# Kernel tuning notes

Hardware: AMD Instinct MI355X
Metric: run time of the kernel (lower is better)

Reference implementation:

```python
import jax, jax.numpy as jnp
import numpy as np

B, T, E, H = 4, 1024, 1024, 16
HS = E // H  # 64
EPS = 1e-5


def layernorm(x, g, b):
    mu = jnp.mean(x, axis=-1, keepdims=True)
    var = jnp.mean((x - mu) ** 2, axis=-1, keepdims=True)
    return (x - mu) * jax.lax.rsqrt(var + EPS) * g + b


def setup_inputs() -> dict:
    key = jax.random.key(0)
    ks = jax.random.split(key, 10)
    s = 0.02
    return {
        "v": jax.random.normal(ks[0], (B, T, E), jnp.float32),
        "k": jax.random.normal(ks[1], (B, T, E), jnp.float32),
        "q": jax.random.normal(ks[2], (B, T, E), jnp.float32),
        "ln_g": jnp.ones((E,), jnp.float32),
        "ln_b": jnp.zeros((E,), jnp.float32),
        # per-head projection weights stacked: [E, H, HS] (x @ W form)
        "Wq": jax.random.normal(ks[3], (E, H, HS), jnp.float32) * s,
        "Wk": jax.random.normal(ks[4], (E, H, HS), jnp.float32) * s,
        "Wv": jax.random.normal(ks[5], (E, H, HS), jnp.float32) * s,
        "Wp": jax.random.normal(ks[6], (E, E), jnp.float32) * s,
        "bp": jnp.zeros((E,), jnp.float32),
    }


def reference(v, k, q, ln_g, ln_b, Wq, Wk, Wv, Wp, bp):
    # shared LayerNorm applied to all three streams
    vn = layernorm(v, ln_g, ln_b)
    kn = layernorm(k, ln_g, ln_b)
    qn = layernorm(q, ln_g, ln_b)
    # batched per-head projections: [B,T,E] x [E,H,HS] -> [B,H,T,HS]
    qh = jnp.einsum("bte,ehd->bhtd", qn, Wq)
    kh = jnp.einsum("bte,ehd->bhtd", kn, Wk)
    vh = jnp.einsum("bte,ehd->bhtd", vn, Wv)
    # NOTE: original scales by C^-0.5 where C = embedding_dim (not head_size)
    scale = jnp.float32(E) ** -0.5
    scores = jnp.einsum("bhtd,bhsd->bhts", qh, kh) * scale  # [B,H,T,T]
    causal = jnp.tril(jnp.ones((T, T), bool))
    scores = jnp.where(causal, scores, jnp.finfo(scores.dtype).min)
    w = jax.nn.softmax(scores, axis=-1)
    out = jnp.einsum("bhts,bhsd->bhtd", w, vh)  # [B,H,T,HS]
    out = out.transpose(0, 2, 1, 3).reshape(B, T, E)  # concat heads
    return out @ Wp + bp
```

## Files before the change

kernel.cpp:

```cpp
#include <hip/hip_runtime.h>
#include <stdint.h>

#define B_ 4
#define T_ 1024
#define E_ 1024
#define H_ 16
#define HS_ 64
#define BT_ 4096

typedef unsigned short u16;
typedef __attribute__((ext_vector_type(8))) short bf16x8;
typedef __attribute__((ext_vector_type(4))) float f32x4;

__device__ __forceinline__ u16 f2bf(float f) {
    unsigned u = __float_as_uint(f);
    u += 0x7fff + ((u >> 16) & 1);
    return (u16)(u >> 16);
}

__device__ __forceinline__ void gll16(const void* g, void* l) {
    __builtin_amdgcn_global_load_lds(
        (const __attribute__((address_space(1))) unsigned int*)g,
        (__attribute__((address_space(3))) unsigned int*)l, 16, 0, 0);
}

__global__ __launch_bounds__(256) void ln_all(
    const float* __restrict__ v, const float* __restrict__ k,
    const float* __restrict__ q, const float* __restrict__ g,
    const float* __restrict__ b,
    u16* __restrict__ vn, u16* __restrict__ kn, u16* __restrict__ qn)
{
    int row = blockIdx.x;
    int which = row >> 12;
    int r = row & 4095;
    const float* src = which == 0 ? v : which == 1 ? k : q;
    u16* dst = which == 0 ? vn : which == 1 ? kn : qn;

    int t = threadIdx.x;
    float4 x = ((const float4*)(src + (size_t)r * E_))[t];
    float s  = x.x + x.y + x.z + x.w;
    float ss = x.x * x.x + x.y * x.y + x.z * x.z + x.w * x.w;
    for (int off = 32; off; off >>= 1) {
        s  += __shfl_down(s, off, 64);
        ss += __shfl_down(ss, off, 64);
    }
    __shared__ float red[8];
    int w = t >> 6, l = t & 63;
    if (l == 0) { red[w] = s; red[4 + w] = ss; }
    __syncthreads();
    float fs  = red[0] + red[1] + red[2] + red[3];
    float fss = red[4] + red[5] + red[6] + red[7];
    float mu  = fs * (1.0f / E_);
    float var = fss * (1.0f / E_) - mu * mu;
    float rstd = rsqrtf(var + 1e-5f);

    float4 gg = ((const float4*)g)[t];
    float4 bb = ((const float4*)b)[t];
    ushort4 o;
    o.x = f2bf((x.x - mu) * rstd * gg.x + bb.x);
    o.y = f2bf((x.y - mu) * rstd * gg.y + bb.y);
    o.z = f2bf((x.z - mu) * rstd * gg.z + bb.z);
    o.w = f2bf((x.w - mu) * rstd * gg.w + bb.w);
    ((ushort4*)(dst + (size_t)r * E_))[t] = o;
}

__global__ __launch_bounds__(256) void wcast_t(
    const float* __restrict__ wq, const float* __restrict__ wk,
    const float* __restrict__ wv, const float* __restrict__ wp,
    u16* __restrict__ tq, u16* __restrict__ tk,
    u16* __restrict__ tv, u16* __restrict__ tp)
{
    int z = blockIdx.z;
    const float* src = z == 0 ? wq : z == 1 ? wk : z == 2 ? wv : wp;
    u16* dst = z == 0 ? tq : z == 1 ? tk : z == 2 ? tv : tp;
    __shared__ float tile[32][33];
    int n0 = blockIdx.x * 32, k0 = blockIdx.y * 32;
    int tx = threadIdx.x & 31, ty = threadIdx.x >> 5;
    for (int i = 0; i < 4; i++)
        tile[ty + i * 8][tx] = src[(size_t)(k0 + ty + i * 8) * E_ + n0 + tx];
    __syncthreads();
    for (int i = 0; i < 4; i++)
        dst[(size_t)(n0 + ty + i * 8) * E_ + k0 + tx] = f2bf(tile[tx][ty + i * 8]);
}

__global__ __launch_bounds__(256) void gemm64(
    const u16* __restrict__ X0, const u16* __restrict__ X1, const u16* __restrict__ X2,
    const u16* __restrict__ W0, const u16* __restrict__ W1, const u16* __restrict__ W2,
    u16* __restrict__ qh, u16* __restrict__ kh, u16* __restrict__ vt,
    float* __restrict__ outF, const float* __restrict__ bias, int fin)
{
    __shared__ __attribute__((aligned(16))) char smem[24576];
    int z = blockIdx.z;
    int mode = fin ? 3 : z;
    const u16* X  = z == 0 ? X0 : z == 1 ? X1 : X2;
    const u16* Wt = z == 0 ? W0 : z == 1 ? W1 : W2;

    const int K = 1024;
    int n0 = blockIdx.x * 128, m0 = blockIdx.y * 64;
    int t = threadIdx.x, w = t >> 6, l = t & 63;
    int lr = l & 15, lg = l >> 4, wm = w >> 1, wn = w & 1;

    f32x4 acc[2][4];
    f32x4 zero = {0.f, 0.f, 0.f, 0.f};
    for (int i = 0; i < 2; i++)
        for (int j = 0; j < 4; j++) acc[i][j] = zero;

    const char* Xb = (const char*)X + (size_t)m0 * 2048;
    const char* Wb = (const char*)Wt + (size_t)n0 * 2048;

    int srow = l >> 2;
    int scol = ((l & 3) ^ ((l >> 3) & 3)) * 16;
    int arow = w * 16 + srow;
    int brow0 = (w * 2) * 16 + srow;
    int brow1 = (w * 2 + 1) * 16 + srow;

    auto stage = [&](int k0, int buf) {
        int kb = k0 * 2;
        gll16(Xb + (size_t)arow * 2048 + kb + scol,
              smem + buf * 4096 + w * 1024 + l * 16);
        gll16(Wb + (size_t)brow0 * 2048 + kb + scol,
              smem + 8192 + buf * 8192 + (w * 2) * 1024 + l * 16);
        gll16(Wb + (size_t)brow1 * 2048 + kb + scol,
              smem + 8192 + buf * 8192 + (w * 2 + 1) * 1024 + l * 16);
    };

    stage(0, 0);
    __syncthreads();
    int b = 0;
    int swr = (lr >> 1) & 3;
    for (int k0 = 0; k0 < K; k0 += 32) {
        if (k0 + 32 < K) stage(k0 + 32, b ^ 1);
        const u16* As = (const u16*)(smem + b * 4096);
        const u16* Bs = (const u16*)(smem + 8192 + b * 8192);
        bf16x8 af[2], bfr[4];
        for (int i = 0; i < 2; i++)
            af[i] = *(const bf16x8*)&As[(wm * 32 + i * 16 + lr) * 32 + (lg ^ swr) * 8];
        for (int j = 0; j < 4; j++)
            bfr[j] = *(const bf16x8*)&Bs[(wn * 64 + j * 16 + lr) * 32 + (lg ^ swr) * 8];
        for (int i = 0; i < 2; i++)
            for (int j = 0; j < 4; j++)
                acc[i][j] = __builtin_amdgcn_mfma_f32_16x16x32_bf16(
                    af[i], bfr[j], acc[i][j], 0, 0, 0);
        __syncthreads();
        b ^= 1;
    }

    if (mode == 3) {
        for (int i = 0; i < 2; i++)
            for (int j = 0; j < 4; j++)
                for (int r = 0; r < 4; r++) {
                    int row = m0 + wm * 32 + i * 16 + lg * 4 + r;
                    int col = n0 + wn * 64 + j * 16 + lr;
                    outF[(size_t)row * E_ + col] = acc[i][j][r] + bias[col];
                }
    } else if (mode < 2) {
        u16* outB = mode == 0 ? qh : kh;
        float sc = mode == 0 ? 0.03125f : 1.0f;
        for (int i = 0; i < 2; i++)
            for (int j = 0; j < 4; j++)
                for (int r = 0; r < 4; r++) {
                    int row = m0 + wm * 32 + i * 16 + lg * 4 + r;
                    int col = n0 + wn * 64 + j * 16 + lr;
                    int bb = row >> 10, tt = row & 1023;
                    int hh = col >> 6, dd = col & 63;
                    outB[(((size_t)(bb * H_ + hh)) * T_ + tt) * HS_ + dd] =
                        f2bf(acc[i][j][r] * sc);
                }
    } else {
        __syncthreads();
        u16* Tt = (u16*)smem + w * 2560;
        for (int i = 0; i < 2; i++)
            for (int j = 0; j < 4; j++)
                for (int r = 0; r < 4; r++)
                    Tt[(j * 16 + lr) * 40 + i * 16 + lg * 4 + r] = f2bf(acc[i][j][r]);
        int bb = m0 >> 10;
        int tbase = (m0 & 1023) + wm * 32;
        int hh = (n0 + wn * 64) >> 6;
        u16* outV = vt + ((size_t)(bb * H_ + hh)) * HS_ * T_;
        int dl = l >> 2, tc = l & 3;
        for (int u = 0; u < 4; u++) {
            int d = u * 16 + dl;
            bf16x8 vv = *(const bf16x8*)&Tt[d * 40 + tc * 8];
            *(bf16x8*)&outV[(size_t)d * T_ + tbase + tc * 8] = vv;
        }
    }
}

__global__ __launch_bounds__(256) void attn(
    const u16* __restrict__ Qh, const u16* __restrict__ Kh,
    const u16* __restrict__ Vt, u16* __restrict__ Out)
{
    int qt = 15 - blockIdx.x;
    int bh = blockIdx.y;
    int b = bh >> 4, h = bh & 15;
    int t = threadIdx.x, w = t >> 6, l = t & 63;
    int lr = l & 15, lg = l >> 4;
    int sw = lr & 7;

    __shared__ __attribute__((aligned(16))) u16 Ks[2][4096];
    __shared__ __attribute__((aligned(16))) u16 Vs[2][4096];
    __shared__ __attribute__((aligned(16))) u16 Ps[4][1024];

    const char* Kb = (const char*)(Kh + (size_t)bh * T_ * HS_);
    const char* Vb = (const char*)(Vt + (size_t)bh * HS_ * T_);
    const u16*  Qb = Qh + (size_t)bh * T_ * HS_;

    int ris = l >> 3;
    int csw = (l & 7) ^ ris;

    int qrow = qt * 64 + w * 16 + lr;
    bf16x8 qf0 = *(const bf16x8*)&Qb[qrow * 64 + lg * 8];
    bf16x8 qf1 = *(const bf16x8*)&Qb[qrow * 64 + 32 + lg * 8];

    f32x4 zero = {0.f, 0.f, 0.f, 0.f};
    f32x4 o[4];
    float m[4], psum[4];
    for (int i = 0; i < 4; i++) o[i] = zero;
    for (int r = 0; r < 4; r++) { m[r] = -1e30f; psum[r] = 0.f; }

    int nkv = qt + 1;

    auto stageKV = [&](int kt2, int bsel) {
        int kv0 = kt2 * 64;
        for (int j = 0; j < 2; j++) {
            int seg = w * 2 + j;
            int row = seg * 8 + ris;
            gll16(Kb + (size_t)(kv0 + row) * 128 + csw * 16,
                  (char*)Ks[bsel] + seg * 1024);
            gll16(Vb + (size_t)row * 2048 + (size_t)kv0 * 2 + csw * 16,
                  (char*)Vs[bsel] + seg * 1024);
        }
    };

    stageKV(0, 0);
    __syncthreads();
    int bsel = 0;

    for (int kt = 0; kt < nkv; kt++) {
        if (kt + 1 < nkv) stageKV(kt + 1, bsel ^ 1);

        int kv0 = kt * 64;
        const u16* Kl = Ks[bsel];
        const u16* Vl = Vs[bsel];

        f32x4 s[4];
        __builtin_amdgcn_s_setprio(1);
        for (int kf = 0; kf < 4; kf++) {
            int key = kf * 16 + lr;
            bf16x8 bk0 = *(const bf16x8*)&Kl[key * 64 + (lg ^ sw) * 8];
            bf16x8 bk1 = *(const bf16x8*)&Kl[key * 64 + ((lg + 4) ^ sw) * 8];
            s[kf] = __builtin_amdgcn_mfma_f32_16x16x32_bf16(qf0, bk0, zero, 0, 0, 0);
            s[kf] = __builtin_amdgcn_mfma_f32_16x16x32_bf16(qf1, bk1, s[kf], 0, 0, 0);
        }
        __builtin_amdgcn_s_setprio(0);

        if (kt == qt) {
            for (int kf = 0; kf < 4; kf++)
                for (int r = 0; r < 4; r++) {
                    int key = kv0 + kf * 16 + lr;
                    int qr  = qt * 64 + w * 16 + lg * 4 + r;
                    if (key > qr) s[kf][r] = -1e30f;
                }
        }

        float pmr[4];
        for (int r = 0; r < 4; r++)
            pmr[r] = fmaxf(fmaxf(s[0][r], s[1][r]), fmaxf(s[2][r], s[3][r]));
        bool ok = (pmr[0] <= m[0] + 8.f) & (pmr[1] <= m[1] + 8.f) &
                  (pmr[2] <= m[2] + 8.f) & (pmr[3] <= m[3] + 8.f);
        if (!__all(ok)) {
            for (int r = 0; r < 4; r++) {
                float mt = pmr[r];
                for (int off = 1; off < 16; off <<= 1)
                    mt = fmaxf(mt, __shfl_xor(mt, off, 64));
                float mn = fmaxf(m[r], mt);
                float al = __expf(m[r] - mn);
                m[r] = mn;
                psum[r] *= al;
                for (int nf = 0; nf < 4; nf++) o[nf][r] *= al;
            }
        }

        for (int kf = 0; kf < 4; kf++)
            for (int r = 0; r < 4; r++) {
                float p = __expf(s[kf][r] - m[r]);
                psum[r] += p;
                int row = lg * 4 + r;
                int ch  = (kf * 2 + (lr >> 3)) ^ (row & 7);
                Ps[w][row * 64 + ch * 8 + sw] = f2bf(p);
            }

        __builtin_amdgcn_s_setprio(1);
        for (int ks = 0; ks < 2; ks++) {
            bf16x8 pa = *(const bf16x8*)&Ps[w][lr * 64 + ((ks * 4 + lg) ^ sw) * 8];
            for (int nf = 0; nf < 4; nf++) {
                int d = nf * 16 + lr;
                bf16x8 bv = *(const bf16x8*)&Vl[d * 64 + ((ks * 4 + lg) ^ sw) * 8];
                o[nf] = __builtin_amdgcn_mfma_f32_16x16x32_bf16(pa, bv, o[nf], 0, 0, 0);
            }
        }
        __builtin_amdgcn_s_setprio(0);
        __syncthreads();
        bsel ^= 1;
    }

    for (int r = 0; r < 4; r++)
        for (int off = 1; off < 16; off <<= 1)
            psum[r] += __shfl_xor(psum[r], off, 64);

    for (int nf = 0; nf < 4; nf++)
        for (int r = 0; r < 4; r++) {
            int row = qt * 64 + w * 16 + lg * 4 + r;
            int col = h * 64 + nf * 16 + lr;
            Out[((size_t)(b * T_ + row)) * E_ + col] = f2bf(o[nf][r] / psum[r]);
        }
}

extern "C" void kernel_launch(void* const* d_in, const int* in_sizes, int n_in,
                              void* d_out, int out_size, void* d_ws, size_t ws_size,
                              hipStream_t stream) {
    const float* v  = (const float*)d_in[0];
    const float* k  = (const float*)d_in[1];
    const float* q  = (const float*)d_in[2];
    const float* g  = (const float*)d_in[3];
    const float* be = (const float*)d_in[4];
    const float* Wq = (const float*)d_in[5];
    const float* Wk = (const float*)d_in[6];
    const float* Wv = (const float*)d_in[7];
    const float* Wp = (const float*)d_in[8];
    const float* bp = (const float*)d_in[9];
    float* out = (float*)d_out;

    char* ws = (char*)d_ws;
    u16* qh  = (u16*)(ws);
    u16* kh  = (u16*)(ws + (8u  << 20));
    u16* vt  = (u16*)(ws + (16u << 20));
    u16* qn  = (u16*)(ws + (24u << 20));
    u16* kn  = (u16*)(ws + (32u << 20));
    u16* vn  = (u16*)(ws + (40u << 20));
    u16* wtq = (u16*)(ws + (48u << 20));
    u16* wtk = (u16*)(ws + (50u << 20));
    u16* wtv = (u16*)(ws + (52u << 20));
    u16* wtp = (u16*)(ws + (54u << 20));
    u16* ao  = (u16*)(ws + (24u << 20));

    hipLaunchKernelGGL(wcast_t, dim3(32, 32, 4), dim3(256), 0, stream,
                       Wq, Wk, Wv, Wp, wtq, wtk, wtv, wtp);
    hipLaunchKernelGGL(ln_all, dim3(3 * BT_), dim3(256), 0, stream,
                       v, k, q, g, be, vn, kn, qn);
    hipLaunchKernelGGL(gemm64, dim3(8, 64, 3), dim3(256), 0, stream,
                       qn, kn, vn, wtq, wtk, wtv, qh, kh, vt,
                       (float*)nullptr, (const float*)nullptr, 0);
    hipLaunchKernelGGL(attn, dim3(16, 64), dim3(256), 0, stream,
                       qh, kh, vt, ao);
    hipLaunchKernelGGL(gemm64, dim3(8, 64, 1), dim3(256), 0, stream,
                       ao, ao, ao, wtp, wtp, wtp,
                       (u16*)nullptr, (u16*)nullptr, (u16*)nullptr, out, bp, 1);
}
```

Baseline: 237.9 us.

## Enlarge GEMM tiles to 128x128, double attention query tile, swizzle block order

The projection GEMM now computes 128x128 output tiles per block instead of 64x128, which doubles the reuse of each staged weight tile and halves the grid. The attention kernel handles 128 query rows per block, with each wave holding two 16-row query fragments, so every staged K/V tile feeds twice as many MFMAs. Both kernels remap block IDs through a swizzle to improve L2 locality. In exchange, register pressure and LDS use rise, the grids shrink (possibly underfilling the CUs), and causal load balance becomes coarser.

```diff
diff --git a/kernel.cpp b/kernel.cpp
--- a/kernel.cpp
+++ b/kernel.cpp
@@ -83,45 +83,49 @@
         dst[(size_t)(n0 + ty + i * 8) * E_ + k0 + tx] = f2bf(tile[tx][ty + i * 8]);
 }
 
-__global__ __launch_bounds__(256) void gemm64(
+__global__ __launch_bounds__(256) void gemm128(
     const u16* __restrict__ X0, const u16* __restrict__ X1, const u16* __restrict__ X2,
     const u16* __restrict__ W0, const u16* __restrict__ W1, const u16* __restrict__ W2,
     u16* __restrict__ qh, u16* __restrict__ kh, u16* __restrict__ vt,
     float* __restrict__ outF, const float* __restrict__ bias, int fin)
 {
-    __shared__ __attribute__((aligned(16))) char smem[24576];
-    int z = blockIdx.z;
-    int mode = fin ? 3 : z;
-    const u16* X  = z == 0 ? X0 : z == 1 ? X1 : X2;
-    const u16* Wt = z == 0 ? W0 : z == 1 ? W1 : W2;
+    __shared__ __attribute__((aligned(16))) char smem[36864];
+    int lid = blockIdx.x + 8 * (blockIdx.y + 32 * blockIdx.z);
+    int cpx = fin ? 32 : 96;
+    int swz = (lid & 7) * cpx + (lid >> 3);
+    int bx = swz & 7;
+    int by = (swz >> 3) & 31;
+    int bz = swz >> 8;
+
+    int mode = fin ? 3 : bz;
+    const u16* X  = bz == 0 ? X0 : bz == 1 ? X1 : X2;
+    const u16* Wt = bz == 0 ? W0 : bz == 1 ? W1 : W2;
 
     const int K = 1024;
-    int n0 = blockIdx.x * 128, m0 = blockIdx.y * 64;
+    int n0 = bx * 128, m0 = by * 128;
     int t = threadIdx.x, w = t >> 6, l = t & 63;
     int lr = l & 15, lg = l >> 4, wm = w >> 1, wn = w & 1;
 
-    f32x4 acc[2][4];
+    f32x4 acc[4][4];
     f32x4 zero = {0.f, 0.f, 0.f, 0.f};
-    for (int i = 0; i < 2; i++)
+    for (int i = 0; i < 4; i++)
         for (int j = 0; j < 4; j++) acc[i][j] = zero;
 
     const char* Xb = (const char*)X + (size_t)m0 * 2048;
     const char* Wb = (const char*)Wt + (size_t)n0 * 2048;
 
-    int srow = l >> 2;
     int scol = ((l & 3) ^ ((l >> 3) & 3)) * 16;
-    int arow = w * 16 + srow;
-    int brow0 = (w * 2) * 16 + srow;
-    int brow1 = (w * 2 + 1) * 16 + srow;
 
     auto stage = [&](int k0, int buf) {
         int kb = k0 * 2;
-        gll16(Xb + (size_t)arow * 2048 + kb + scol,
-              smem + buf * 4096 + w * 1024 + l * 16);
-        gll16(Wb + (size_t)brow0 * 2048 + kb + scol,
-              smem + 8192 + buf * 8192 + (w * 2) * 1024 + l * 16);
-        gll16(Wb + (size_t)brow1 * 2048 + kb + scol,
-              smem + 8192 + buf * 8192 + (w * 2 + 1) * 1024 + l * 16);
+        for (int j = 0; j < 2; j++) {
+            int seg = w * 2 + j;
+            int row = seg * 16 + (l >> 2);
+            gll16(Xb + (size_t)row * 2048 + kb + scol,
+                  smem + buf * 8192 + seg * 1024 + l * 16);
+            gll16(Wb + (size_t)row * 2048 + kb + scol,
+                  smem + 16384 + buf * 8192 + seg * 1024 + l * 16);
+        }
     };
 
     stage(0, 0);
@@ -130,14 +134,14 @@
     int swr = (lr >> 1) & 3;
     for (int k0 = 0; k0 < K; k0 += 32) {
         if (k0 + 32 < K) stage(k0 + 32, b ^ 1);
-        const u16* As = (const u16*)(smem + b * 4096);
-        const u16* Bs = (const u16*)(smem + 8192 + b * 8192);
-        bf16x8 af[2], bfr[4];
-        for (int i = 0; i < 2; i++)
-            af[i] = *(const bf16x8*)&As[(wm * 32 + i * 16 + lr) * 32 + (lg ^ swr) * 8];
+        const u16* As = (const u16*)(smem + b * 8192);
+        const u16* Bs = (const u16*)(smem + 16384 + b * 8192);
+        bf16x8 af[4], bfr[4];
+        for (int i = 0; i < 4; i++)
+            af[i] = *(const bf16x8*)&As[(wm * 64 + i * 16 + lr) * 32 + (lg ^ swr) * 8];
         for (int j = 0; j < 4; j++)
             bfr[j] = *(const bf16x8*)&Bs[(wn * 64 + j * 16 + lr) * 32 + (lg ^ swr) * 8];
-        for (int i = 0; i < 2; i++)
+        for (int i = 0; i < 4; i++)
             for (int j = 0; j < 4; j++)
                 acc[i][j] = __builtin_amdgcn_mfma_f32_16x16x32_bf16(
                     af[i], bfr[j], acc[i][j], 0, 0, 0);
@@ -146,20 +150,20 @@
     }
 
     if (mode == 3) {
-        for (int i = 0; i < 2; i++)
+        for (int i = 0; i < 4; i++)
             for (int j = 0; j < 4; j++)
                 for (int r = 0; r < 4; r++) {
-                    int row = m0 + wm * 32 + i * 16 + lg * 4 + r;
+                    int row = m0 + wm * 64 + i * 16 + lg * 4 + r;
                     int col = n0 + wn * 64 + j * 16 + lr;
                     outF[(size_t)row * E_ + col] = acc[i][j][r] + bias[col];
                 }
     } else if (mode < 2) {
         u16* outB = mode == 0 ? qh : kh;
         float sc = mode == 0 ? 0.03125f : 1.0f;
-        for (int i = 0; i < 2; i++)
+        for (int i = 0; i < 4; i++)
             for (int j = 0; j < 4; j++)
                 for (int r = 0; r < 4; r++) {
-                    int row = m0 + wm * 32 + i * 16 + lg * 4 + r;
+                    int row = m0 + wm * 64 + i * 16 + lg * 4 + r;
                     int col = n0 + wn * 64 + j * 16 + lr;
                     int bb = row >> 10, tt = row & 1023;
                     int hh = col >> 6, dd = col & 63;
@@ -167,20 +171,19 @@
                         f2bf(acc[i][j][r] * sc);
                 }
     } else {
-        __syncthreads();
-        u16* Tt = (u16*)smem + w * 2560;
-        for (int i = 0; i < 2; i++)
+        u16* Tt = (u16*)smem + w * 4608;
+        for (int i = 0; i < 4; i++)
             for (int j = 0; j < 4; j++)
                 for (int r = 0; r < 4; r++)
-                    Tt[(j * 16 + lr) * 40 + i * 16 + lg * 4 + r] = f2bf(acc[i][j][r]);
+                    Tt[(j * 16 + lr) * 72 + i * 16 + lg * 4 + r] = f2bf(acc[i][j][r]);
         int bb = m0 >> 10;
-        int tbase = (m0 & 1023) + wm * 32;
+        int tbase = (m0 & 1023) + wm * 64;
         int hh = (n0 + wn * 64) >> 6;
         u16* outV = vt + ((size_t)(bb * H_ + hh)) * HS_ * T_;
-        int dl = l >> 2, tc = l & 3;
-        for (int u = 0; u < 4; u++) {
-            int d = u * 16 + dl;
-            bf16x8 vv = *(const bf16x8*)&Tt[d * 40 + tc * 8];
+        int dl = l >> 3, tc = l & 7;
+        for (int u = 0; u < 8; u++) {
+            int d = u * 8 + dl;
+            bf16x8 vv = *(const bf16x8*)&Tt[d * 72 + tc * 8];
             *(bf16x8*)&outV[(size_t)d * T_ + tbase + tc * 8] = vv;
         }
     }
@@ -190,8 +193,10 @@
     const u16* __restrict__ Qh, const u16* __restrict__ Kh,
     const u16* __restrict__ Vt, u16* __restrict__ Out)
 {
-    int qt = 15 - blockIdx.x;
-    int bh = blockIdx.y;
+    int lid = blockIdx.x + 8 * blockIdx.y;
+    int swz = (lid & 7) * 64 + (lid >> 3);
+    int qt = 7 - (swz & 7);
+    int bh = swz >> 3;
     int b = bh >> 4, h = bh & 15;
     int t = threadIdx.x, w = t >> 6, l = t & 63;
     int lr = l & 15, lg = l >> 4;
@@ -199,7 +204,7 @@
 
     __shared__ __attribute__((aligned(16))) u16 Ks[2][4096];
     __shared__ __attribute__((aligned(16))) u16 Vs[2][4096];
-    __shared__ __attribute__((aligned(16))) u16 Ps[4][1024];
+    __shared__ __attribute__((aligned(16))) u16 Ps[4][2048];
 
     const char* Kb = (const char*)(Kh + (size_t)bh * T_ * HS_);
     const char* Vb = (const char*)(Vt + (size_t)bh * HS_ * T_);
@@ -208,17 +213,22 @@
     int ris = l >> 3;
     int csw = (l & 7) ^ ris;
 
-    int qrow = qt * 64 + w * 16 + lr;
-    bf16x8 qf0 = *(const bf16x8*)&Qb[qrow * 64 + lg * 8];
-    bf16x8 qf1 = *(const bf16x8*)&Qb[qrow * 64 + 32 + lg * 8];
+    bf16x8 qf[2][2];
+    for (int i = 0; i < 2; i++) {
+        int qrow = qt * 128 + w * 32 + i * 16 + lr;
+        qf[i][0] = *(const bf16x8*)&Qb[qrow * 64 + lg * 8];
+        qf[i][1] = *(const bf16x8*)&Qb[qrow * 64 + 32 + lg * 8];
+    }
 
     f32x4 zero = {0.f, 0.f, 0.f, 0.f};
-    f32x4 o[4];
-    float m[4], psum[4];
-    for (int i = 0; i < 4; i++) o[i] = zero;
-    for (int r = 0; r < 4; r++) { m[r] = -1e30f; psum[r] = 0.f; }
-
-    int nkv = qt + 1;
+    f32x4 o[2][4];
+    float m[2][4], psum[2][4];
+    for (int i = 0; i < 2; i++)
+        for (int nf = 0; nf < 4; nf++) o[i][nf] = zero;
+    for (int i = 0; i < 2; i++)
+        for (int r = 0; r < 4; r++) { m[i][r] = -1e30f; psum[i][r] = 0.f; }
+
+    int nkv = 2 * qt + 2;
 
     auto stageKV = [&](int kt2, int bsel) {
         int kv0 = kt2 * 64;
@@ -243,60 +253,70 @@
         const u16* Kl = Ks[bsel];
         const u16* Vl = Vs[bsel];
 
-        f32x4 s[4];
+        f32x4 s[2][4];
         __builtin_amdgcn_s_setprio(1);
         for (int kf = 0; kf < 4; kf++) {
             int key = kf * 16 + lr;
             bf16x8 bk0 = *(const bf16x8*)&Kl[key * 64 + (lg ^ sw) * 8];
             bf16x8 bk1 = *(const bf16x8*)&Kl[key * 64 + ((lg + 4) ^ sw) * 8];
-            s[kf] = __builtin_amdgcn_mfma_f32_16x16x32_bf16(qf0, bk0, zero, 0, 0, 0);
-            s[kf] = __builtin_amdgcn_mfma_f32_16x16x32_bf16(qf1, bk1, s[kf], 0, 0, 0);
+            for (int i = 0; i < 2; i++) {
+                s[i][kf] = __builtin_amdgcn_mfma_f32_16x16x32_bf16(qf[i][0], bk0, zero, 0, 0, 0);
+                s[i][kf] = __builtin_amdgcn_mfma_f32_16x16x32_bf16(qf[i][1], bk1, s[i][kf], 0, 0, 0);
+            }
         }
         __builtin_amdgcn_s_setprio(0);
 
-        if (kt == qt) {
+        if (kt >= 2 * qt) {
+            for (int i = 0; i < 2; i++)
+                for (int kf = 0; kf < 4; kf++)
+                    for (int r = 0; r < 4; r++) {
+                        int key = kv0 + kf * 16 + lr;
+                        int qr  = qt * 128 + w * 32 + i * 16 + lg * 4 + r;
+                        if (key > qr) s[i][kf][r] = -1e30f;
+                    }
+        }
+
+        float pmr[2][4];
+        bool ok = true;
+        for (int i = 0; i < 2; i++)
+            for (int r = 0; r < 4; r++) {
+                pmr[i][r] = fmaxf(fmaxf(s[i][0][r], s[i][1][r]),
+                                  fmaxf(s[i][2][r], s[i][3][r]));
+                ok &= (pmr[i][r] <= m[i][r] + 8.f);
+            }
+        if (!__all(ok)) {
+            for (int i = 0; i < 2; i++)
+                for (int r = 0; r < 4; r++) {
+                    float mt = pmr[i][r];
+                    for (int off = 1; off < 16; off <<= 1)
+                        mt = fmaxf(mt, __shfl_xor(mt, off, 64));
+                    float mn = fmaxf(m[i][r], mt);
+                    float al = __expf(m[i][r] - mn);
+                    m[i][r] = mn;
+                    psum[i][r] *= al;
+                    for (int nf = 0; nf < 4; nf++) o[i][nf][r] *= al;
+                }
+        }
+
+        for (int i = 0; i < 2; i++)
             for (int kf = 0; kf < 4; kf++)
                 for (int r = 0; r < 4; r++) {
-                    int key = kv0 + kf * 16 + lr;
-                    int qr  = qt * 64 + w * 16 + lg * 4 + r;
-                    if (key > qr) s[kf][r] = -1e30f;
+                    float p = __expf(s[i][kf][r] - m[i][r]);
+                    psum[i][r] += p;
+                    int row = i * 16 + lg * 4 + r;
+                    int ch  = (kf * 2 + (lr >> 3)) ^ (row & 7);
+                    Ps[w][row * 64 + ch * 8 + sw] = f2bf(p);
                 }
-        }
-
-        float pmr[4];
-        for (int r = 0; r < 4; r++)
-            pmr[r] = fmaxf(fmaxf(s[0][r], s[1][r]), fmaxf(s[2][r], s[3][r]));
-        bool ok = (pmr[0] <= m[0] + 8.f) & (pmr[1] <= m[1] + 8.f) &
-                  (pmr[2] <= m[2] + 8.f) & (pmr[3] <= m[3] + 8.f);
-        if (!__all(ok)) {
-            for (int r = 0; r < 4; r++) {
-                float mt = pmr[r];
-                for (int off = 1; off < 16; off <<= 1)
-                    mt = fmaxf(mt, __shfl_xor(mt, off, 64));
-                float mn = fmaxf(m[r], mt);
-                float al = __expf(m[r] - mn);
-                m[r] = mn;
-                psum[r] *= al;
-                for (int nf = 0; nf < 4; nf++) o[nf][r] *= al;
-            }
-        }
-
-        for (int kf = 0; kf < 4; kf++)
-            for (int r = 0; r < 4; r++) {
-                float p = __expf(s[kf][r] - m[r]);
-                psum[r] += p;
-                int row = lg * 4 + r;
-                int ch  = (kf * 2 + (lr >> 3)) ^ (row & 7);
-                Ps[w][row * 64 + ch * 8 + sw] = f2bf(p);
-            }
 
         __builtin_amdgcn_s_setprio(1);
         for (int ks = 0; ks < 2; ks++) {
-            bf16x8 pa = *(const bf16x8*)&Ps[w][lr * 64 + ((ks * 4 + lg) ^ sw) * 8];
+            bf16x8 pa0 = *(const bf16x8*)&Ps[w][(lr) * 64 + ((ks * 4 + lg) ^ sw) * 8];
+            bf16x8 pa1 = *(const bf16x8*)&Ps[w][(16 + lr) * 64 + ((ks * 4 + lg) ^ sw) * 8];
             for (int nf = 0; nf < 4; nf++) {
                 int d = nf * 16 + lr;
                 bf16x8 bv = *(const bf16x8*)&Vl[d * 64 + ((ks * 4 + lg) ^ sw) * 8];
-                o[nf] = __builtin_amdgcn_mfma_f32_16x16x32_bf16(pa, bv, o[nf], 0, 0, 0);
+                o[0][nf] = __builtin_amdgcn_mfma_f32_16x16x32_bf16(pa0, bv, o[0][nf], 0, 0, 0);
+                o[1][nf] = __builtin_amdgcn_mfma_f32_16x16x32_bf16(pa1, bv, o[1][nf], 0, 0, 0);
             }
         }
         __builtin_amdgcn_s_setprio(0);
@@ -304,16 +324,18 @@
         bsel ^= 1;
     }
 
-    for (int r = 0; r < 4; r++)
-        for (int off = 1; off < 16; off <<= 1)
-            psum[r] += __shfl_xor(psum[r], off, 64);
-
-    for (int nf = 0; nf < 4; nf++)
-        for (int r = 0; r < 4; r++) {
-            int row = qt * 64 + w * 16 + lg * 4 + r;
-            int col = h * 64 + nf * 16 + lr;
-            Out[((size_t)(b * T_ + row)) * E_ + col] = f2bf(o[nf][r] / psum[r]);
-        }
+    for (int i = 0; i < 2; i++)
+        for (int r = 0; r < 4; r++)
+            for (int off = 1; off < 16; off <<= 1)
+                psum[i][r] += __shfl_xor(psum[i][r], off, 64);
+
+    for (int i = 0; i < 2; i++)
+        for (int nf = 0; nf < 4; nf++)
+            for (int r = 0; r < 4; r++) {
+                int row = qt * 128 + w * 32 + i * 16 + lg * 4 + r;
+                int col = h * 64 + nf * 16 + lr;
+                Out[((size_t)(b * T_ + row)) * E_ + col] = f2bf(o[i][nf][r] / psum[i][r]);
+            }
 }
 
 extern "C" void kernel_launch(void* const* d_in, const int* in_sizes, int n_in,
@@ -348,12 +370,12 @@
                        Wq, Wk, Wv, Wp, wtq, wtk, wtv, wtp);
     hipLaunchKernelGGL(ln_all, dim3(3 * BT_), dim3(256), 0, stream,
                        v, k, q, g, be, vn, kn, qn);
-    hipLaunchKernelGGL(gemm64, dim3(8, 64, 3), dim3(256), 0, stream,
+    hipLaunchKernelGGL(gemm128, dim3(8, 32, 3), dim3(256), 0, stream,
                        qn, kn, vn, wtq, wtk, wtv, qh, kh, vt,
                        (float*)nullptr, (const float*)nullptr, 0);
-    hipLaunchKernelGGL(attn, dim3(16, 64), dim3(256), 0, stream,
+    hipLaunchKernelGGL(attn, dim3(8, 64), dim3(256), 0, stream,
                        qh, kh, vt, ao);
-    hipLaunchKernelGGL(gemm64, dim3(8, 64, 1), dim3(256), 0, stream,
+    hipLaunchKernelGGL(gemm128, dim3(8, 32, 1), dim3(256), 0, stream,
                        ao, ao, ao, wtp, wtp, wtp,
                        (u16*)nullptr, (u16*)nullptr, (u16*)nullptr, out, bp, 1);
 }
```

Result: faster. 211.5 us (-11.1%).
